# Kernel optimization log

Hardware: AMD Instinct MI355X
Metric: run time of the kernel (lower is better)

Reference implementation:

```python
import jax, jax.numpy as jnp
import numpy as np

N, IN_RAW, H, E, UNROLLS = 1024, 10, 96, 16384, 2

def _p(key, shape):
    return jax.random.normal(key, shape, dtype=jnp.float32) * 0.05

def setup_inputs() -> dict:
    key = jax.random.key(0)
    ks = jax.random.split(key, 24)
    x = jax.random.normal(ks[0], (N, IN_RAW), dtype=jnp.float32)
    edge_index = jax.random.randint(ks[1], (2, E), 0, N, dtype=jnp.int64)
    adj = jax.random.randint(ks[2], (N, N), 0, 2, dtype=jnp.int32)
    return {
        'x': x, 'edge_index': edge_index, 'adj': adj,
        # init_layer
        'W_init': _p(ks[3], (H, IN_RAW - 1)), 'b_init': _p(ks[4], (H,)),
        # GatedGraphConv (num_layers=1): weight [H,H], GRUCell params
        'W_ggc': _p(ks[5], (H, H)),
        'W_ih': _p(ks[6], (3 * H, H)), 'W_hh': _p(ks[7], (3 * H, H)),
        'b_ih': _p(ks[8], (3 * H,)), 'b_hh': _p(ks[9], (3 * H,)),
        # edge_attention: Linear(2H->H), Linear(H->1)
        'Wa1': _p(ks[10], (H, 2 * H)), 'ba1': _p(ks[11], (H,)),
        'Wa2': _p(ks[12], (1, H)), 'ba2': _p(ks[13], (1,)),
        # out MLP
        'Wo1': _p(ks[14], (H, H)), 'bo1': _p(ks[15], (H,)),
        'Wo2': _p(ks[16], (H, H)), 'bo2': _p(ks[17], (H,)),
        # heads
        'Wp1': _p(ks[18], (1, H)), 'bp1': _p(ks[19], (1,)),
        'Wp2': _p(ks[20], (1, H)), 'bp2': _p(ks[21], (1,)),
    }

def _leaky(v):
    return jnp.where(v >= 0, v, 0.01 * v)  # LeakyReLU default slope

def _ggnn_forward(x, edge_index, adj,
                  W_init, b_init, W_ggc, W_ih, W_hh, b_ih, b_hh,
                  Wa1, ba1, Wa2, ba2, Wo1, bo1, Wo2, bo2,
                  Wp1, bp1, Wp2, bp2):
    src, tgt = edge_index[0], edge_index[1]
    x = x[:, :-1]                                   # data.x[:, :-1]
    x = _leaky(x @ W_init.T + b_init)               # [N,H]
    adj_mask = (adj == 1)
    for _ in range(UNROLLS):
        # GatedGraphConv, 1 layer, aggr='mean'
        m = x @ W_ggc                               # [N,H]
        s = jax.ops.segment_sum(m[src], tgt, num_segments=N)
        cnt = jax.ops.segment_sum(jnp.ones((E,), x.dtype), tgt, num_segments=N)
        agg = s / jnp.maximum(cnt, 1.0)[:, None]    # mean, 0 for isolated nodes
        # GRUCell(agg, x)
        gi = agg @ W_ih.T + b_ih
        gh = x @ W_hh.T + b_hh
        ir, iz, inn = jnp.split(gi, 3, axis=1)
        hr, hz, hn = jnp.split(gh, 3, axis=1)
        r = jax.nn.sigmoid(ir + hr)
        z = jax.nn.sigmoid(iz + hz)
        n = jnp.tanh(inn + r * hn)
        x = (1.0 - z) * n + z * x
        # edge attention: concat(x_i, x_j) -> Linear(2H->H) decomposed into
        # two [H,H] halves so the NxNx2H concat tensor is never materialized.
        hi = x @ Wa1[:, :H].T                       # acts on t1 (row i)
        hj = x @ Wa1[:, H:].T                       # acts on t2 (row j)
        h = jax.nn.sigmoid(hi[:, None, :] + hj[None, :, :] + ba1)  # [N,N,H]
        coeffs = jax.nn.sigmoid(h @ Wa2[0] + ba2[0])               # [N,N]
        coeffs = jnp.where(adj_mask, coeffs, 0.0)
        x = coeffs @ x
    x = _leaky(x @ Wo1.T + bo1)
    x = _leaky(x @ Wo2.T + bo2)
    out1 = jax.nn.sigmoid(x @ Wp1.T + bp1)
    out2 = jax.nn.sigmoid(x @ Wp2.T + bp2)
    return out1, out2

def reference(x, edge_index, adj,
              W_init, b_init, W_ggc, W_ih, W_hh, b_ih, b_hh,
              Wa1, ba1, Wa2, ba2, Wo1, bo1, Wo2, bo2,
              Wp1, bp1, Wp2, bp2):
    return _ggnn_forward(x, edge_index, adj,
                         W_init, b_init, W_ggc, W_ih, W_hh, b_ih, b_hh,
                         Wa1, ba1, Wa2, ba2, Wo1, bo1, Wo2, bo2,
                         Wp1, bp1, Wp2, bp2)
```

## Files before the change

### kernel.cpp

```cpp
#include <hip/hip_runtime.h>

#define Nn 1024
#define Hh 96
#define Ee 16384
#define IN_K 9
#define IN_STRIDE 10
#define NH (Nn * Hh)
#define XS 128
#define SLOTS 64

__device__ __forceinline__ float sigf(float v) {
    return __builtin_amdgcn_rcpf(1.0f + __expf(-v));
}
__device__ __forceinline__ float tanhfast(float v) {
    float e = __expf(2.0f * v);
    return (e - 1.0f) * __builtin_amdgcn_rcpf(e + 1.0f);
}
__device__ __forceinline__ float leakyf(float v) {
    return v >= 0.0f ? v : 0.01f * v;
}

__global__ __launch_bounds__(256) void setup_kernel(
    const float* __restrict__ W_hh, const float* __restrict__ Wa1,
    const float* __restrict__ Wo1, const float* __restrict__ Wo2,
    const float* __restrict__ W_ggc, const float* __restrict__ W_ih,
    const float* __restrict__ x_in, const float* __restrict__ W_init,
    const float* __restrict__ b_init,
    float* __restrict__ Wt_hh, float* __restrict__ Wt_a1i,
    float* __restrict__ Wt_a1j, float* __restrict__ Wt_o1,
    float* __restrict__ Wt_o2, float* __restrict__ Wf,
    int* __restrict__ deg, float* __restrict__ xA)
{
    int gt = blockIdx.x * 256 + threadIdx.x;
    if (gt < Nn) deg[gt] = 0;
    if (gt < 64512) {
        int idx = gt;
        if (idx < 27648) {
            int k = idx / 288, c = idx % 288;
            Wt_hh[idx] = W_hh[c * 96 + k];
        } else if ((idx -= 27648) < 9216) {
            int k = idx / 96, h = idx % 96;
            Wt_a1i[idx] = Wa1[h * 192 + k];
        } else if ((idx -= 9216) < 9216) {
            int k = idx / 96, h = idx % 96;
            Wt_a1j[idx] = Wa1[h * 192 + 96 + k];
        } else if ((idx -= 9216) < 9216) {
            int k = idx / 96, j = idx % 96;
            Wt_o1[idx] = Wo1[j * 96 + k];
        } else {
            idx -= 9216;
            int k = idx / 96, j = idx % 96;
            Wt_o2[idx] = Wo2[j * 96 + k];
        }
    }
    if (gt < 27648) {
        int k = gt / 288, c = gt % 288;
        const float* g = W_ggc + k * 96;
        const float* w = W_ih + c * 96;
        float acc = 0.0f;
        for (int j = 0; j < 96; ++j) acc += g[j] * w[j];
        Wf[gt] = acc;
    }
    if (gt < NH) {
        int n = gt / Hh, j = gt - n * Hh;
        const float* xr = x_in + n * IN_STRIDE;
        const float* wr = W_init + j * IN_K;
        float acc = b_init[j];
#pragma unroll
        for (int k = 0; k < IN_K; ++k) acc += xr[k] * wr[k];
        xA[n * XS + j] = leakyf(acc);
    }
}

__global__ __launch_bounds__(256) void edges_kernel(
    const int* __restrict__ ei, int* __restrict__ deg, int* __restrict__ bucket)
{
    int e = blockIdx.x * 256 + threadIdx.x;
    if (e >= Ee) return;
    int src = ei[e];
    int tgt = ei[Ee + e];
    int slot = atomicAdd(&deg[tgt], 1);
    if (slot < SLOTS) bucket[tgt * SLOTS + slot] = src;
}

__global__ __launch_bounds__(384, 4) void gru_kernel(
    const float* __restrict__ xA, const int* __restrict__ deg,
    const int* __restrict__ bucket,
    const float* __restrict__ Wf, const float* __restrict__ Wt_hh,
    const float* __restrict__ b_ih, const float* __restrict__ b_hh,
    const float* __restrict__ Wt_a1i, const float* __restrict__ Wt_a1j,
    const float* __restrict__ ba1,
    float* __restrict__ xB, float* __restrict__ Ei, float* __restrict__ EjT)
{
    __shared__ float Pq[4][Hh];
    __shared__ float Pm[Hh];
    __shared__ float Xr[Hh];
    __shared__ float Xo[Hh];
    __shared__ float red6[4][Hh][6];
    __shared__ float redp[4][Hh][2];
    int tid = threadIdx.x;
    int q = tid / Hh;
    int h = tid - q * Hh;
    int n = blockIdx.x;
    {
        int d = deg[n];
        int dc = d < SLOTS ? d : SLOTS;
        const int* bk = bucket + n * SLOTS;
        float acc = 0.0f;
        for (int s = q; s < dc; s += 4)
            acc += xA[bk[s] * XS + h];
        Pq[q][h] = acc;
        if (q == 0) Xr[h] = xA[n * XS + h];
    }
    __syncthreads();
    if (q == 0) {
        float inv = __builtin_amdgcn_rcpf(fmaxf((float)deg[n], 1.0f));
        Pm[h] = (Pq[0][h] + Pq[1][h] + Pq[2][h] + Pq[3][h]) * inv;
    }
    __syncthreads();
    {
        const float* pf = Wf + h;
        const float* ph = Wt_hh + h;
        float gir = 0.f, giz = 0.f, gin = 0.f;
        float ghr = 0.f, ghz = 0.f, ghn = 0.f;
        int k0 = q * 24;
#pragma unroll 4
        for (int k = k0; k < k0 + 24; ++k) {
            float a = Pm[k];
            float xv = Xr[k];
            int o = k * 288;
            gir += a * pf[o];
            giz += a * pf[o + 96];
            gin += a * pf[o + 192];
            ghr += xv * ph[o];
            ghz += xv * ph[o + 96];
            ghn += xv * ph[o + 192];
        }
        red6[q][h][0] = gir;
        red6[q][h][1] = giz;
        red6[q][h][2] = gin;
        red6[q][h][3] = ghr;
        red6[q][h][4] = ghz;
        red6[q][h][5] = ghn;
    }
    __syncthreads();
    if (q == 0) {
        float gir = b_ih[h], giz = b_ih[Hh + h], gin = b_ih[2 * Hh + h];
        float ghr = b_hh[h], ghz = b_hh[Hh + h], ghn = b_hh[2 * Hh + h];
#pragma unroll
        for (int qq = 0; qq < 4; ++qq) {
            gir += red6[qq][h][0];
            giz += red6[qq][h][1];
            gin += red6[qq][h][2];
            ghr += red6[qq][h][3];
            ghz += red6[qq][h][4];
            ghn += red6[qq][h][5];
        }
        float rr = sigf(gir + ghr);
        float z = sigf(giz + ghz);
        float nn2 = tanhfast(gin + rr * ghn);
        float xo = (1.0f - z) * nn2 + z * Xr[h];
        xB[n * XS + h] = xo;
        Xo[h] = xo;
    }
    __syncthreads();
    {
        const float* wi = Wt_a1i + h;
        const float* wj = Wt_a1j + h;
        float a = 0.0f, bb = 0.0f;
        int k0 = q * 24;
#pragma unroll 4
        for (int k = k0; k < k0 + 24; ++k) {
            float xv = Xo[k];
            a += xv * wi[k * 96];
            bb += xv * wj[k * 96];
        }
        redp[q][h][0] = a;
        redp[q][h][1] = bb;
    }
    __syncthreads();
    if (q == 0) {
        float a = redp[0][h][0] + redp[1][h][0] + redp[2][h][0] + redp[3][h][0];
        float bb = redp[0][h][1] + redp[1][h][1] + redp[2][h][1] + redp[3][h][1];
        Ei[n * Hh + h] = __expf(-(a + ba1[h]));
        EjT[h * Nn + n] = __expf(-bb);
    }
}

__global__ __launch_bounds__(1024) void attn_kernel_u0(
    const float* __restrict__ Ei, const float* __restrict__ EjT,
    const float* __restrict__ Wa2, const float* __restrict__ ba2,
    const int* __restrict__ adj, const float* __restrict__ xB,
    float* __restrict__ xOut)
{
    __shared__ float sm[7168];
    int tid = threadIdx.x;
    int i0 = blockIdx.x * 4;
    {
        int j = tid;
        int m0 = adj[(i0 + 0) * Nn + j];
        int m1 = adj[(i0 + 1) * Nn + j];
        int m2 = adj[(i0 + 2) * Nn + j];
        int m3 = adj[(i0 + 3) * Nn + j];
        const float* e0 = Ei + i0 * Hh;
        float s0 = 0.f, s1 = 0.f, s2 = 0.f, s3 = 0.f;
#pragma unroll 8
        for (int k = 0; k < Hh; ++k) {
            float e = EjT[k * Nn + j];
            float wk = Wa2[k];
            s0 += __builtin_amdgcn_rcpf(fmaf(e0[k], e, 1.0f)) * wk;
            s1 += __builtin_amdgcn_rcpf(fmaf(e0[96 + k], e, 1.0f)) * wk;
            s2 += __builtin_amdgcn_rcpf(fmaf(e0[192 + k], e, 1.0f)) * wk;
            s3 += __builtin_amdgcn_rcpf(fmaf(e0[288 + k], e, 1.0f)) * wk;
        }
        float b2 = ba2[0];
        sm[0 * Nn + j] = (m0 == 1) ? sigf(s0 + b2) : 0.0f;
        sm[1 * Nn + j] = (m1 == 1) ? sigf(s1 + b2) : 0.0f;
        sm[2 * Nn + j] = (m2 == 1) ? sigf(s2 + b2) : 0.0f;
        sm[3 * Nn + j] = (m3 == 1) ? sigf(s3 + b2) : 0.0f;
    }
    __syncthreads();
    {
        int q = tid >> 7;
        int h = tid & 127;
        if (h < Hh) {
            int jb = q * 128;
            const float* xc = xB + jb * XS + h;
            const float* c0 = sm + 0 * Nn + jb;
            const float* c1 = sm + 1 * Nn + jb;
            const float* c2 = sm + 2 * Nn + jb;
            const float* c3 = sm + 3 * Nn + jb;
            float a0 = 0.f, a1 = 0.f, a2 = 0.f, a3 = 0.f;
#pragma unroll 4
            for (int j = 0; j < 128; ++j) {
                float xv = xc[j * XS];
                a0 += c0[j] * xv;
                a1 += c1[j] * xv;
                a2 += c2[j] * xv;
                a3 += c3[j] * xv;
            }
            sm[4096 + ((q * 4 + 0) * Hh) + h] = a0;
            sm[4096 + ((q * 4 + 1) * Hh) + h] = a1;
            sm[4096 + ((q * 4 + 2) * Hh) + h] = a2;
            sm[4096 + ((q * 4 + 3) * Hh) + h] = a3;
        }
    }
    __syncthreads();
    if (tid < 4 * Hh) {
        int r = tid / Hh, h = tid - r * Hh;
        float v = 0.f;
#pragma unroll
        for (int q = 0; q < 8; ++q)
            v += sm[4096 + ((q * 4 + r) * Hh) + h];
        xOut[(i0 + r) * XS + h] = v;
    }
}

__global__ __launch_bounds__(1024) void attn_kernel_u1(
    const float* __restrict__ Ei, const float* __restrict__ EjT,
    const float* __restrict__ Wa2, const float* __restrict__ ba2,
    const int* __restrict__ adj, const float* __restrict__ xB,
    const float* __restrict__ Wt_o1, const float* __restrict__ bo1,
    const float* __restrict__ Wt_o2, const float* __restrict__ bo2,
    const float* __restrict__ Wp1, const float* __restrict__ bp1,
    const float* __restrict__ Wp2, const float* __restrict__ bp2,
    float* __restrict__ out)
{
    __shared__ float sm[7168];
    __shared__ float hd[3][4][Hh];
    int tid = threadIdx.x;
    int i0 = blockIdx.x * 4;
    {
        int j = tid;
        int m0 = adj[(i0 + 0) * Nn + j];
        int m1 = adj[(i0 + 1) * Nn + j];
        int m2 = adj[(i0 + 2) * Nn + j];
        int m3 = adj[(i0 + 3) * Nn + j];
        const float* e0 = Ei + i0 * Hh;
        float s0 = 0.f, s1 = 0.f, s2 = 0.f, s3 = 0.f;
#pragma unroll 8
        for (int k = 0; k < Hh; ++k) {
            float e = EjT[k * Nn + j];
            float wk = Wa2[k];
            s0 += __builtin_amdgcn_rcpf(fmaf(e0[k], e, 1.0f)) * wk;
            s1 += __builtin_amdgcn_rcpf(fmaf(e0[96 + k], e, 1.0f)) * wk;
            s2 += __builtin_amdgcn_rcpf(fmaf(e0[192 + k], e, 1.0f)) * wk;
            s3 += __builtin_amdgcn_rcpf(fmaf(e0[288 + k], e, 1.0f)) * wk;
        }
        float b2 = ba2[0];
        sm[0 * Nn + j] = (m0 == 1) ? sigf(s0 + b2) : 0.0f;
        sm[1 * Nn + j] = (m1 == 1) ? sigf(s1 + b2) : 0.0f;
        sm[2 * Nn + j] = (m2 == 1) ? sigf(s2 + b2) : 0.0f;
        sm[3 * Nn + j] = (m3 == 1) ? sigf(s3 + b2) : 0.0f;
    }
    __syncthreads();
    {
        int q = tid >> 7;
        int h = tid & 127;
        if (h < Hh) {
            int jb = q * 128;
            const float* xc = xB + jb * XS + h;
            const float* c0 = sm + 0 * Nn + jb;
            const float* c1 = sm + 1 * Nn + jb;
            const float* c2 = sm + 2 * Nn + jb;
            const float* c3 = sm + 3 * Nn + jb;
            float a0 = 0.f, a1 = 0.f, a2 = 0.f, a3 = 0.f;
#pragma unroll 4
            for (int j = 0; j < 128; ++j) {
                float xv = xc[j * XS];
                a0 += c0[j] * xv;
                a1 += c1[j] * xv;
                a2 += c2[j] * xv;
                a3 += c3[j] * xv;
            }
            sm[4096 + ((q * 4 + 0) * Hh) + h] = a0;
            sm[4096 + ((q * 4 + 1) * Hh) + h] = a1;
            sm[4096 + ((q * 4 + 2) * Hh) + h] = a2;
            sm[4096 + ((q * 4 + 3) * Hh) + h] = a3;
        }
    }
    __syncthreads();
    if (tid < 4 * Hh) {
        int r = tid / Hh, h = tid - r * Hh;
        float v = 0.f;
#pragma unroll
        for (int q = 0; q < 8; ++q)
            v += sm[4096 + ((q * 4 + r) * Hh) + h];
        hd[0][r][h] = v;
    }
    __syncthreads();
    if (tid < 4 * Hh) {
        int r = tid / Hh, h = tid - r * Hh;
        const float* w = Wt_o1 + h;
        const float* xr = hd[0][r];
        float acc = bo1[h];
        for (int k = 0; k < Hh; ++k) acc += xr[k] * w[k * 96];
        hd[1][r][h] = leakyf(acc);
    }
    __syncthreads();
    if (tid < 4 * Hh) {
        int r = tid / Hh, h = tid - r * Hh;
        const float* w = Wt_o2 + h;
        const float* xr = hd[1][r];
        float acc = bo2[h];
        for (int k = 0; k < Hh; ++k) acc += xr[k] * w[k * 96];
        hd[2][r][h] = leakyf(acc);
    }
    __syncthreads();
    if (tid < 8) {
        int r = tid >> 1, which = tid & 1;
        const float* wp = which ? Wp2 : Wp1;
        const float* xr = hd[2][r];
        float acc = 0.f;
        for (int k = 0; k < Hh; ++k) acc += xr[k] * wp[k];
        float b = which ? bp2[0] : bp1[0];
        out[which * Nn + i0 + r] = sigf(acc + b);
    }
}

extern "C" void kernel_launch(void* const* d_in, const int* in_sizes, int n_in,
                              void* d_out, int out_size, void* d_ws, size_t ws_size,
                              hipStream_t stream)
{
    const float* x_in   = (const float*)d_in[0];
    const int*   ei     = (const int*)d_in[1];
    const int*   adj    = (const int*)d_in[2];
    const float* W_init = (const float*)d_in[3];
    const float* b_init = (const float*)d_in[4];
    const float* W_ggc  = (const float*)d_in[5];
    const float* W_ih   = (const float*)d_in[6];
    const float* W_hh   = (const float*)d_in[7];
    const float* b_ih   = (const float*)d_in[8];
    const float* b_hh   = (const float*)d_in[9];
    const float* Wa1    = (const float*)d_in[10];
    const float* ba1    = (const float*)d_in[11];
    const float* Wa2    = (const float*)d_in[12];
    const float* ba2    = (const float*)d_in[13];
    const float* Wo1    = (const float*)d_in[14];
    const float* bo1    = (const float*)d_in[15];
    const float* Wo2    = (const float*)d_in[16];
    const float* bo2    = (const float*)d_in[17];
    const float* Wp1    = (const float*)d_in[18];
    const float* bp1    = (const float*)d_in[19];
    const float* Wp2    = (const float*)d_in[20];
    const float* bp2    = (const float*)d_in[21];
    float* out = (float*)d_out;

    float* ws     = (float*)d_ws;
    float* xA     = ws;
    float* xB     = xA + Nn * XS;
    float* xC     = xB + Nn * XS;
    float* Ei     = xC + Nn * XS;
    float* EjT    = Ei + NH;
    float* Wt_hh  = EjT + NH;
    float* Wf     = Wt_hh + 27648;
    float* Wt_a1i = Wf + 27648;
    float* Wt_a1j = Wt_a1i + 9216;
    float* Wt_o1  = Wt_a1j + 9216;
    float* Wt_o2  = Wt_o1 + 9216;
    int*   deg    = (int*)(Wt_o2 + 9216);
    int*   bucket = deg + Nn;

    setup_kernel<<<(NH + 255) / 256, 256, 0, stream>>>(
        W_hh, Wa1, Wo1, Wo2, W_ggc, W_ih, x_in, W_init, b_init,
        Wt_hh, Wt_a1i, Wt_a1j, Wt_o1, Wt_o2, Wf, deg, xA);
    edges_kernel<<<(Ee + 255) / 256, 256, 0, stream>>>(ei, deg, bucket);

    gru_kernel<<<Nn, 384, 0, stream>>>(
        xA, deg, bucket, Wf, Wt_hh, b_ih, b_hh, Wt_a1i, Wt_a1j, ba1,
        xB, Ei, EjT);
    attn_kernel_u0<<<Nn / 4, 1024, 0, stream>>>(
        Ei, EjT, Wa2, ba2, adj, xB, xC);
    gru_kernel<<<Nn, 384, 0, stream>>>(
        xC, deg, bucket, Wf, Wt_hh, b_ih, b_hh, Wt_a1i, Wt_a1j, ba1,
        xB, Ei, EjT);
    attn_kernel_u1<<<Nn / 4, 1024, 0, stream>>>(
        Ei, EjT, Wa2, ba2, adj, xB,
        Wt_o1, bo1, Wt_o2, bo2, Wp1, bp1, Wp2, bp2, out);
}
```

Baseline: 192.7 us.

## Fuse all stages into one persistent kernel with global atomic barriers

Replaces the six separate launches (setup, edge bucketing, two GRU and two attention kernels) with a single 256-block persistent kernel that separates phases with atomic grid-wide barriers. The GRU phase now processes four nodes per block so each weight load is reused across four rows, and edge bucketing runs in one block using LDS atomics. This removes launch gaps and inter-kernel drain, at the cost of relying on all 256 blocks being co-resident, using only 384 of 1024 threads in the GRU phase, and adding a memset launch to reset the barrier counters.

```diff
diff --git a/kernel.cpp b/kernel.cpp
--- a/kernel.cpp
+++ b/kernel.cpp
@@ -8,6 +8,7 @@
 #define NH (Nn * Hh)
 #define XS 128
 #define SLOTS 64
+#define NBLK 256
 
 __device__ __forceinline__ float sigf(float v) {
     return __builtin_amdgcn_rcpf(1.0f + __expf(-v));
@@ -20,204 +21,189 @@
     return v >= 0.0f ? v : 0.01f * v;
 }
 
-__global__ __launch_bounds__(256) void setup_kernel(
-    const float* __restrict__ W_hh, const float* __restrict__ Wa1,
-    const float* __restrict__ Wo1, const float* __restrict__ Wo2,
-    const float* __restrict__ W_ggc, const float* __restrict__ W_ih,
-    const float* __restrict__ x_in, const float* __restrict__ W_init,
-    const float* __restrict__ b_init,
-    float* __restrict__ Wt_hh, float* __restrict__ Wt_a1i,
-    float* __restrict__ Wt_a1j, float* __restrict__ Wt_o1,
-    float* __restrict__ Wt_o2, float* __restrict__ Wf,
-    int* __restrict__ deg, float* __restrict__ xA)
-{
-    int gt = blockIdx.x * 256 + threadIdx.x;
-    if (gt < Nn) deg[gt] = 0;
-    if (gt < 64512) {
-        int idx = gt;
-        if (idx < 27648) {
-            int k = idx / 288, c = idx % 288;
-            Wt_hh[idx] = W_hh[c * 96 + k];
-        } else if ((idx -= 27648) < 9216) {
-            int k = idx / 96, h = idx % 96;
-            Wt_a1i[idx] = Wa1[h * 192 + k];
-        } else if ((idx -= 9216) < 9216) {
-            int k = idx / 96, h = idx % 96;
-            Wt_a1j[idx] = Wa1[h * 192 + 96 + k];
-        } else if ((idx -= 9216) < 9216) {
-            int k = idx / 96, j = idx % 96;
-            Wt_o1[idx] = Wo1[j * 96 + k];
-        } else {
-            idx -= 9216;
-            int k = idx / 96, j = idx % 96;
-            Wt_o2[idx] = Wo2[j * 96 + k];
-        }
-    }
-    if (gt < 27648) {
-        int k = gt / 288, c = gt % 288;
-        const float* g = W_ggc + k * 96;
-        const float* w = W_ih + c * 96;
+struct Params {
+    const float* x_in; const int* ei; const int* adj;
+    const float* W_init; const float* b_init;
+    const float* W_ggc; const float* W_ih; const float* W_hh;
+    const float* b_ih; const float* b_hh;
+    const float* Wa1; const float* ba1; const float* Wa2; const float* ba2;
+    const float* Wo1; const float* bo1; const float* Wo2; const float* bo2;
+    const float* Wp1; const float* bp1; const float* Wp2; const float* bp2;
+    float* out;
+    float* xA; float* xB; float* xC; float* Ei; float* EjT;
+    float* Wt_hh; float* Wf; float* Wt_a1i; float* Wt_a1j;
+    float* Wt_o1; float* Wt_o2;
+    int* deg; int* bucket; int* bar;
+};
+
+union Shm {
+    struct {
+        float Pm[4][Hh];
+        float Xr[4][Hh];
+        float Xo[4][Hh];
+        float red[4][4][6][Hh];
+        float redp[4][4][2][Hh];
+    } g;
+    struct {
+        float sm[7168];
+        float hd[3][4][Hh];
+    } a;
+    int ldeg[Nn];
+};
+
+__device__ __forceinline__ void gsync(int* bar, int idx) {
+    __syncthreads();
+    if (threadIdx.x == 0) {
+        __threadfence();
+        __hip_atomic_fetch_add(bar + idx, 1, __ATOMIC_ACQ_REL,
+                               __HIP_MEMORY_SCOPE_AGENT);
+        while (__hip_atomic_load(bar + idx, __ATOMIC_ACQUIRE,
+                                 __HIP_MEMORY_SCOPE_AGENT) < NBLK) {
+            __builtin_amdgcn_s_sleep(1);
+        }
+    }
+    __syncthreads();
+}
+
+__device__ __forceinline__ void gru_phase(const Params& p, Shm& sh,
+                                          const float* xin, float* xout)
+{
+    int tid = threadIdx.x;
+    int i0 = blockIdx.x * 4;
+    int h = tid % Hh;
+    int q = tid / Hh;
+    bool act = tid < 4 * Hh;
+
+    if (act) {
+        int n = i0 + q;
+        int d = p.deg[n];
+        int dc = d < SLOTS ? d : SLOTS;
+        const int* bk = p.bucket + n * SLOTS;
         float acc = 0.0f;
-        for (int j = 0; j < 96; ++j) acc += g[j] * w[j];
-        Wf[gt] = acc;
-    }
-    if (gt < NH) {
-        int n = gt / Hh, j = gt - n * Hh;
-        const float* xr = x_in + n * IN_STRIDE;
-        const float* wr = W_init + j * IN_K;
-        float acc = b_init[j];
-#pragma unroll
-        for (int k = 0; k < IN_K; ++k) acc += xr[k] * wr[k];
-        xA[n * XS + j] = leakyf(acc);
-    }
-}
-
-__global__ __launch_bounds__(256) void edges_kernel(
-    const int* __restrict__ ei, int* __restrict__ deg, int* __restrict__ bucket)
-{
-    int e = blockIdx.x * 256 + threadIdx.x;
-    if (e >= Ee) return;
-    int src = ei[e];
-    int tgt = ei[Ee + e];
-    int slot = atomicAdd(&deg[tgt], 1);
-    if (slot < SLOTS) bucket[tgt * SLOTS + slot] = src;
-}
-
-__global__ __launch_bounds__(384, 4) void gru_kernel(
-    const float* __restrict__ xA, const int* __restrict__ deg,
-    const int* __restrict__ bucket,
-    const float* __restrict__ Wf, const float* __restrict__ Wt_hh,
-    const float* __restrict__ b_ih, const float* __restrict__ b_hh,
-    const float* __restrict__ Wt_a1i, const float* __restrict__ Wt_a1j,
-    const float* __restrict__ ba1,
-    float* __restrict__ xB, float* __restrict__ Ei, float* __restrict__ EjT)
-{
-    __shared__ float Pq[4][Hh];
-    __shared__ float Pm[Hh];
-    __shared__ float Xr[Hh];
-    __shared__ float Xo[Hh];
-    __shared__ float red6[4][Hh][6];
-    __shared__ float redp[4][Hh][2];
-    int tid = threadIdx.x;
-    int q = tid / Hh;
-    int h = tid - q * Hh;
-    int n = blockIdx.x;
-    {
-        int d = deg[n];
-        int dc = d < SLOTS ? d : SLOTS;
-        const int* bk = bucket + n * SLOTS;
-        float acc = 0.0f;
-        for (int s = q; s < dc; s += 4)
-            acc += xA[bk[s] * XS + h];
-        Pq[q][h] = acc;
-        if (q == 0) Xr[h] = xA[n * XS + h];
-    }
-    __syncthreads();
-    if (q == 0) {
-        float inv = __builtin_amdgcn_rcpf(fmaxf((float)deg[n], 1.0f));
-        Pm[h] = (Pq[0][h] + Pq[1][h] + Pq[2][h] + Pq[3][h]) * inv;
-    }
-    __syncthreads();
-    {
-        const float* pf = Wf + h;
-        const float* ph = Wt_hh + h;
-        float gir = 0.f, giz = 0.f, gin = 0.f;
-        float ghr = 0.f, ghz = 0.f, ghn = 0.f;
+        for (int s = 0; s < dc; ++s)
+            acc += xin[bk[s] * XS + h];
+        float inv = __builtin_amdgcn_rcpf(fmaxf((float)d, 1.0f));
+        sh.g.Pm[q][h] = acc * inv;
+        sh.g.Xr[q][h] = xin[n * XS + h];
+    }
+    __syncthreads();
+
+    if (act) {
+        float g0[4], g1[4], g2[4], g3[4], g4[4], g5[4];
+#pragma unroll
+        for (int r = 0; r < 4; ++r) {
+            g0[r] = g1[r] = g2[r] = g3[r] = g4[r] = g5[r] = 0.0f;
+        }
+        const float* pf = p.Wf + h;
+        const float* ph = p.Wt_hh + h;
         int k0 = q * 24;
 #pragma unroll 4
         for (int k = k0; k < k0 + 24; ++k) {
-            float a = Pm[k];
-            float xv = Xr[k];
             int o = k * 288;
-            gir += a * pf[o];
-            giz += a * pf[o + 96];
-            gin += a * pf[o + 192];
-            ghr += xv * ph[o];
-            ghz += xv * ph[o + 96];
-            ghn += xv * ph[o + 192];
-        }
-        red6[q][h][0] = gir;
-        red6[q][h][1] = giz;
-        red6[q][h][2] = gin;
-        red6[q][h][3] = ghr;
-        red6[q][h][4] = ghz;
-        red6[q][h][5] = ghn;
-    }
-    __syncthreads();
-    if (q == 0) {
-        float gir = b_ih[h], giz = b_ih[Hh + h], gin = b_ih[2 * Hh + h];
-        float ghr = b_hh[h], ghz = b_hh[Hh + h], ghn = b_hh[2 * Hh + h];
+            float w0 = pf[o], w1 = pf[o + 96], w2 = pf[o + 192];
+            float u0 = ph[o], u1 = ph[o + 96], u2 = ph[o + 192];
+#pragma unroll
+            for (int r = 0; r < 4; ++r) {
+                float a  = sh.g.Pm[r][k];
+                float xv = sh.g.Xr[r][k];
+                g0[r] += a * w0;  g1[r] += a * w1;  g2[r] += a * w2;
+                g3[r] += xv * u0; g4[r] += xv * u1; g5[r] += xv * u2;
+            }
+        }
+#pragma unroll
+        for (int r = 0; r < 4; ++r) {
+            sh.g.red[q][r][0][h] = g0[r];
+            sh.g.red[q][r][1][h] = g1[r];
+            sh.g.red[q][r][2][h] = g2[r];
+            sh.g.red[q][r][3][h] = g3[r];
+            sh.g.red[q][r][4][h] = g4[r];
+            sh.g.red[q][r][5][h] = g5[r];
+        }
+    }
+    __syncthreads();
+
+    if (act) {
+        int n = i0 + q;
+        float gir = p.b_ih[h], giz = p.b_ih[Hh + h], gin = p.b_ih[2 * Hh + h];
+        float ghr = p.b_hh[h], ghz = p.b_hh[Hh + h], ghn = p.b_hh[2 * Hh + h];
 #pragma unroll
         for (int qq = 0; qq < 4; ++qq) {
-            gir += red6[qq][h][0];
-            giz += red6[qq][h][1];
-            gin += red6[qq][h][2];
-            ghr += red6[qq][h][3];
-            ghz += red6[qq][h][4];
-            ghn += red6[qq][h][5];
-        }
-        float rr = sigf(gir + ghr);
-        float z = sigf(giz + ghz);
+            gir += sh.g.red[qq][q][0][h];
+            giz += sh.g.red[qq][q][1][h];
+            gin += sh.g.red[qq][q][2][h];
+            ghr += sh.g.red[qq][q][3][h];
+            ghz += sh.g.red[qq][q][4][h];
+            ghn += sh.g.red[qq][q][5][h];
+        }
+        float rr  = sigf(gir + ghr);
+        float z   = sigf(giz + ghz);
         float nn2 = tanhfast(gin + rr * ghn);
-        float xo = (1.0f - z) * nn2 + z * Xr[h];
-        xB[n * XS + h] = xo;
-        Xo[h] = xo;
-    }
-    __syncthreads();
-    {
-        const float* wi = Wt_a1i + h;
-        const float* wj = Wt_a1j + h;
-        float a = 0.0f, bb = 0.0f;
+        float xo  = (1.0f - z) * nn2 + z * sh.g.Xr[q][h];
+        xout[n * XS + h] = xo;
+        sh.g.Xo[q][h] = xo;
+    }
+    __syncthreads();
+
+    if (act) {
+        const float* wi = p.Wt_a1i + h;
+        const float* wj = p.Wt_a1j + h;
+        float pa[4] = {0, 0, 0, 0}, pb[4] = {0, 0, 0, 0};
         int k0 = q * 24;
 #pragma unroll 4
         for (int k = k0; k < k0 + 24; ++k) {
-            float xv = Xo[k];
-            a += xv * wi[k * 96];
-            bb += xv * wj[k * 96];
-        }
-        redp[q][h][0] = a;
-        redp[q][h][1] = bb;
-    }
-    __syncthreads();
-    if (q == 0) {
-        float a = redp[0][h][0] + redp[1][h][0] + redp[2][h][0] + redp[3][h][0];
-        float bb = redp[0][h][1] + redp[1][h][1] + redp[2][h][1] + redp[3][h][1];
-        Ei[n * Hh + h] = __expf(-(a + ba1[h]));
-        EjT[h * Nn + n] = __expf(-bb);
-    }
-}
-
-__global__ __launch_bounds__(1024) void attn_kernel_u0(
-    const float* __restrict__ Ei, const float* __restrict__ EjT,
-    const float* __restrict__ Wa2, const float* __restrict__ ba2,
-    const int* __restrict__ adj, const float* __restrict__ xB,
-    float* __restrict__ xOut)
-{
-    __shared__ float sm[7168];
+            float wik = wi[k * 96], wjk = wj[k * 96];
+#pragma unroll
+            for (int r = 0; r < 4; ++r) {
+                float xv = sh.g.Xo[r][k];
+                pa[r] += xv * wik;
+                pb[r] += xv * wjk;
+            }
+        }
+#pragma unroll
+        for (int r = 0; r < 4; ++r) {
+            sh.g.redp[q][r][0][h] = pa[r];
+            sh.g.redp[q][r][1][h] = pb[r];
+        }
+    }
+    __syncthreads();
+    if (act) {
+        int n = i0 + q;
+        float a = sh.g.redp[0][q][0][h] + sh.g.redp[1][q][0][h]
+                + sh.g.redp[2][q][0][h] + sh.g.redp[3][q][0][h];
+        float b = sh.g.redp[0][q][1][h] + sh.g.redp[1][q][1][h]
+                + sh.g.redp[2][q][1][h] + sh.g.redp[3][q][1][h];
+        p.Ei[n * Hh + h]  = __expf(-(a + p.ba1[h]));
+        p.EjT[h * Nn + n] = __expf(-b);
+    }
+}
+
+__device__ __forceinline__ void attn_coeff(const Params& p, Shm& sh,
+                                           const float* xB)
+{
     int tid = threadIdx.x;
     int i0 = blockIdx.x * 4;
     {
         int j = tid;
-        int m0 = adj[(i0 + 0) * Nn + j];
-        int m1 = adj[(i0 + 1) * Nn + j];
-        int m2 = adj[(i0 + 2) * Nn + j];
-        int m3 = adj[(i0 + 3) * Nn + j];
-        const float* e0 = Ei + i0 * Hh;
+        int m0 = p.adj[(i0 + 0) * Nn + j];
+        int m1 = p.adj[(i0 + 1) * Nn + j];
+        int m2 = p.adj[(i0 + 2) * Nn + j];
+        int m3 = p.adj[(i0 + 3) * Nn + j];
+        const float* e0 = p.Ei + i0 * Hh;
         float s0 = 0.f, s1 = 0.f, s2 = 0.f, s3 = 0.f;
 #pragma unroll 8
         for (int k = 0; k < Hh; ++k) {
-            float e = EjT[k * Nn + j];
-            float wk = Wa2[k];
+            float e = p.EjT[k * Nn + j];
+            float wk = p.Wa2[k];
             s0 += __builtin_amdgcn_rcpf(fmaf(e0[k], e, 1.0f)) * wk;
             s1 += __builtin_amdgcn_rcpf(fmaf(e0[96 + k], e, 1.0f)) * wk;
             s2 += __builtin_amdgcn_rcpf(fmaf(e0[192 + k], e, 1.0f)) * wk;
             s3 += __builtin_amdgcn_rcpf(fmaf(e0[288 + k], e, 1.0f)) * wk;
         }
-        float b2 = ba2[0];
-        sm[0 * Nn + j] = (m0 == 1) ? sigf(s0 + b2) : 0.0f;
-        sm[1 * Nn + j] = (m1 == 1) ? sigf(s1 + b2) : 0.0f;
-        sm[2 * Nn + j] = (m2 == 1) ? sigf(s2 + b2) : 0.0f;
-        sm[3 * Nn + j] = (m3 == 1) ? sigf(s3 + b2) : 0.0f;
+        float b2 = p.ba2[0];
+        sh.a.sm[0 * Nn + j] = (m0 == 1) ? sigf(s0 + b2) : 0.0f;
+        sh.a.sm[1 * Nn + j] = (m1 == 1) ? sigf(s1 + b2) : 0.0f;
+        sh.a.sm[2 * Nn + j] = (m2 == 1) ? sigf(s2 + b2) : 0.0f;
+        sh.a.sm[3 * Nn + j] = (m3 == 1) ? sigf(s3 + b2) : 0.0f;
     }
     __syncthreads();
     {
@@ -226,10 +212,10 @@
         if (h < Hh) {
             int jb = q * 128;
             const float* xc = xB + jb * XS + h;
-            const float* c0 = sm + 0 * Nn + jb;
-            const float* c1 = sm + 1 * Nn + jb;
-            const float* c2 = sm + 2 * Nn + jb;
-            const float* c3 = sm + 3 * Nn + jb;
+            const float* c0 = sh.a.sm + 0 * Nn + jb;
+            const float* c1 = sh.a.sm + 1 * Nn + jb;
+            const float* c2 = sh.a.sm + 2 * Nn + jb;
+            const float* c3 = sh.a.sm + 3 * Nn + jb;
             float a0 = 0.f, a1 = 0.f, a2 = 0.f, a3 = 0.f;
 #pragma unroll 4
             for (int j = 0; j < 128; ++j) {
@@ -239,123 +225,141 @@
                 a2 += c2[j] * xv;
                 a3 += c3[j] * xv;
             }
-            sm[4096 + ((q * 4 + 0) * Hh) + h] = a0;
-            sm[4096 + ((q * 4 + 1) * Hh) + h] = a1;
-            sm[4096 + ((q * 4 + 2) * Hh) + h] = a2;
-            sm[4096 + ((q * 4 + 3) * Hh) + h] = a3;
-        }
-    }
-    __syncthreads();
+            sh.a.sm[4096 + ((q * 4 + 0) * Hh) + h] = a0;
+            sh.a.sm[4096 + ((q * 4 + 1) * Hh) + h] = a1;
+            sh.a.sm[4096 + ((q * 4 + 2) * Hh) + h] = a2;
+            sh.a.sm[4096 + ((q * 4 + 3) * Hh) + h] = a3;
+        }
+    }
+    __syncthreads();
+}
+
+__device__ __forceinline__ void attn_tail_u0(const Params& p, Shm& sh,
+                                             float* xOut)
+{
+    int tid = threadIdx.x;
+    int i0 = blockIdx.x * 4;
     if (tid < 4 * Hh) {
         int r = tid / Hh, h = tid - r * Hh;
         float v = 0.f;
 #pragma unroll
         for (int q = 0; q < 8; ++q)
-            v += sm[4096 + ((q * 4 + r) * Hh) + h];
+            v += sh.a.sm[4096 + ((q * 4 + r) * Hh) + h];
         xOut[(i0 + r) * XS + h] = v;
     }
 }
 
-__global__ __launch_bounds__(1024) void attn_kernel_u1(
-    const float* __restrict__ Ei, const float* __restrict__ EjT,
-    const float* __restrict__ Wa2, const float* __restrict__ ba2,
-    const int* __restrict__ adj, const float* __restrict__ xB,
-    const float* __restrict__ Wt_o1, const float* __restrict__ bo1,
-    const float* __restrict__ Wt_o2, const float* __restrict__ bo2,
-    const float* __restrict__ Wp1, const float* __restrict__ bp1,
-    const float* __restrict__ Wp2, const float* __restrict__ bp2,
-    float* __restrict__ out)
-{
-    __shared__ float sm[7168];
-    __shared__ float hd[3][4][Hh];
+__device__ __forceinline__ void attn_tail_u1(const Params& p, Shm& sh)
+{
     int tid = threadIdx.x;
     int i0 = blockIdx.x * 4;
-    {
-        int j = tid;
-        int m0 = adj[(i0 + 0) * Nn + j];
-        int m1 = adj[(i0 + 1) * Nn + j];
-        int m2 = adj[(i0 + 2) * Nn + j];
-        int m3 = adj[(i0 + 3) * Nn + j];
-        const float* e0 = Ei + i0 * Hh;
-        float s0 = 0.f, s1 = 0.f, s2 = 0.f, s3 = 0.f;
-#pragma unroll 8
-        for (int k = 0; k < Hh; ++k) {
-            float e = EjT[k * Nn + j];
-            float wk = Wa2[k];
-            s0 += __builtin_amdgcn_rcpf(fmaf(e0[k], e, 1.0f)) * wk;
-            s1 += __builtin_amdgcn_rcpf(fmaf(e0[96 + k], e, 1.0f)) * wk;
-            s2 += __builtin_amdgcn_rcpf(fmaf(e0[192 + k], e, 1.0f)) * wk;
-            s3 += __builtin_amdgcn_rcpf(fmaf(e0[288 + k], e, 1.0f)) * wk;
-        }
-        float b2 = ba2[0];
-        sm[0 * Nn + j] = (m0 == 1) ? sigf(s0 + b2) : 0.0f;
-        sm[1 * Nn + j] = (m1 == 1) ? sigf(s1 + b2) : 0.0f;
-        sm[2 * Nn + j] = (m2 == 1) ? sigf(s2 + b2) : 0.0f;
-        sm[3 * Nn + j] = (m3 == 1) ? sigf(s3 + b2) : 0.0f;
-    }
-    __syncthreads();
-    {
-        int q = tid >> 7;
-        int h = tid & 127;
-        if (h < Hh) {
-            int jb = q * 128;
-            const float* xc = xB + jb * XS + h;
-            const float* c0 = sm + 0 * Nn + jb;
-            const float* c1 = sm + 1 * Nn + jb;
-            const float* c2 = sm + 2 * Nn + jb;
-            const float* c3 = sm + 3 * Nn + jb;
-            float a0 = 0.f, a1 = 0.f, a2 = 0.f, a3 = 0.f;
-#pragma unroll 4
-            for (int j = 0; j < 128; ++j) {
-                float xv = xc[j * XS];
-                a0 += c0[j] * xv;
-                a1 += c1[j] * xv;
-                a2 += c2[j] * xv;
-                a3 += c3[j] * xv;
-            }
-            sm[4096 + ((q * 4 + 0) * Hh) + h] = a0;
-            sm[4096 + ((q * 4 + 1) * Hh) + h] = a1;
-            sm[4096 + ((q * 4 + 2) * Hh) + h] = a2;
-            sm[4096 + ((q * 4 + 3) * Hh) + h] = a3;
-        }
-    }
-    __syncthreads();
     if (tid < 4 * Hh) {
         int r = tid / Hh, h = tid - r * Hh;
         float v = 0.f;
 #pragma unroll
         for (int q = 0; q < 8; ++q)
-            v += sm[4096 + ((q * 4 + r) * Hh) + h];
-        hd[0][r][h] = v;
+            v += sh.a.sm[4096 + ((q * 4 + r) * Hh) + h];
+        sh.a.hd[0][r][h] = v;
     }
     __syncthreads();
     if (tid < 4 * Hh) {
         int r = tid / Hh, h = tid - r * Hh;
-        const float* w = Wt_o1 + h;
-        const float* xr = hd[0][r];
-        float acc = bo1[h];
+        const float* w = p.Wt_o1 + h;
+        const float* xr = sh.a.hd[0][r];
+        float acc = p.bo1[h];
         for (int k = 0; k < Hh; ++k) acc += xr[k] * w[k * 96];
-        hd[1][r][h] = leakyf(acc);
+        sh.a.hd[1][r][h] = leakyf(acc);
     }
     __syncthreads();
     if (tid < 4 * Hh) {
         int r = tid / Hh, h = tid - r * Hh;
-        const float* w = Wt_o2 + h;
-        const float* xr = hd[1][r];
-        float acc = bo2[h];
+        const float* w = p.Wt_o2 + h;
+        const float* xr = sh.a.hd[1][r];
+        float acc = p.bo2[h];
         for (int k = 0; k < Hh; ++k) acc += xr[k] * w[k * 96];
-        hd[2][r][h] = leakyf(acc);
+        sh.a.hd[2][r][h] = leakyf(acc);
     }
     __syncthreads();
     if (tid < 8) {
         int r = tid >> 1, which = tid & 1;
-        const float* wp = which ? Wp2 : Wp1;
-        const float* xr = hd[2][r];
+        const float* wp = which ? p.Wp2 : p.Wp1;
+        const float* xr = sh.a.hd[2][r];
         float acc = 0.f;
         for (int k = 0; k < Hh; ++k) acc += xr[k] * wp[k];
-        float b = which ? bp2[0] : bp1[0];
-        out[which * Nn + i0 + r] = sigf(acc + b);
-    }
+        float b = which ? p.bp2[0] : p.bp1[0];
+        p.out[which * Nn + i0 + r] = sigf(acc + b);
+    }
+}
+
+__global__ __launch_bounds__(1024) void fused_kernel(Params p)
+{
+    __shared__ Shm sh;
+    int tid = threadIdx.x;
+    int blk = blockIdx.x;
+
+    if (blk == 0) {
+        sh.ldeg[tid] = 0;
+        __syncthreads();
+        for (int e = tid; e < Ee; e += 1024) {
+            int src = p.ei[e];
+            int tgt = p.ei[Ee + e];
+            int slot = atomicAdd(&sh.ldeg[tgt], 1);
+            if (slot < SLOTS) p.bucket[tgt * SLOTS + slot] = src;
+        }
+        __syncthreads();
+        p.deg[tid] = sh.ldeg[tid];
+    } else {
+        int gt = (blk - 1) * 1024 + tid;
+        if (gt < 64512) {
+            int idx = gt;
+            if (idx < 27648) {
+                int k = idx / 288, c = idx % 288;
+                p.Wt_hh[idx] = p.W_hh[c * 96 + k];
+            } else if ((idx -= 27648) < 9216) {
+                int k = idx / 96, h2 = idx % 96;
+                p.Wt_a1i[idx] = p.Wa1[h2 * 192 + k];
+            } else if ((idx -= 9216) < 9216) {
+                int k = idx / 96, h2 = idx % 96;
+                p.Wt_a1j[idx] = p.Wa1[h2 * 192 + 96 + k];
+            } else if ((idx -= 9216) < 9216) {
+                int k = idx / 96, j = idx % 96;
+                p.Wt_o1[idx] = p.Wo1[j * 96 + k];
+            } else {
+                idx -= 9216;
+                int k = idx / 96, j = idx % 96;
+                p.Wt_o2[idx] = p.Wo2[j * 96 + k];
+            }
+        }
+        if (gt < 27648) {
+            int k = gt / 288, c = gt % 288;
+            const float* g = p.W_ggc + k * 96;
+            const float* w = p.W_ih + c * 96;
+            float acc = 0.0f;
+            for (int j = 0; j < 96; ++j) acc += g[j] * w[j];
+            p.Wf[gt] = acc;
+        }
+        if (gt < NH) {
+            int n = gt / Hh, j = gt - n * Hh;
+            const float* xr = p.x_in + n * IN_STRIDE;
+            const float* wr = p.W_init + j * IN_K;
+            float acc = p.b_init[j];
+#pragma unroll
+            for (int k = 0; k < IN_K; ++k) acc += xr[k] * wr[k];
+            p.xA[n * XS + j] = leakyf(acc);
+        }
+    }
+    gsync(p.bar, 0);
+
+    gru_phase(p, sh, p.xA, p.xB);
+    gsync(p.bar, 1);
+    attn_coeff(p, sh, p.xB);
+    attn_tail_u0(p, sh, p.xC);
+    gsync(p.bar, 2);
+
+    gru_phase(p, sh, p.xC, p.xB);
+    gsync(p.bar, 3);
+    attn_coeff(p, sh, p.xB);
+    attn_tail_u1(p, sh);
 }
 
 extern "C" void kernel_launch(void* const* d_in, const int* in_sizes, int n_in,
@@ -400,21 +404,23 @@
     float* Wt_o2  = Wt_o1 + 9216;
     int*   deg    = (int*)(Wt_o2 + 9216);
     int*   bucket = deg + Nn;
-
-    setup_kernel<<<(NH + 255) / 256, 256, 0, stream>>>(
-        W_hh, Wa1, Wo1, Wo2, W_ggc, W_ih, x_in, W_init, b_init,
-        Wt_hh, Wt_a1i, Wt_a1j, Wt_o1, Wt_o2, Wf, deg, xA);
-    edges_kernel<<<(Ee + 255) / 256, 256, 0, stream>>>(ei, deg, bucket);
-
-    gru_kernel<<<Nn, 384, 0, stream>>>(
-        xA, deg, bucket, Wf, Wt_hh, b_ih, b_hh, Wt_a1i, Wt_a1j, ba1,
-        xB, Ei, EjT);
-    attn_kernel_u0<<<Nn / 4, 1024, 0, stream>>>(
-        Ei, EjT, Wa2, ba2, adj, xB, xC);
-    gru_kernel<<<Nn, 384, 0, stream>>>(
-        xC, deg, bucket, Wf, Wt_hh, b_ih, b_hh, Wt_a1i, Wt_a1j, ba1,
-        xB, Ei, EjT);
-    attn_kernel_u1<<<Nn / 4, 1024, 0, stream>>>(
-        Ei, EjT, Wa2, ba2, adj, xB,
-        Wt_o1, bo1, Wt_o2, bo2, Wp1, bp1, Wp2, bp2, out);
-}
+    int*   bar    = bucket + Nn * SLOTS;
+
+    hipMemsetAsync(bar, 0, 4 * sizeof(int), stream);
+
+    Params p;
+    p.x_in = x_in; p.ei = ei; p.adj = adj;
+    p.W_init = W_init; p.b_init = b_init;
+    p.W_ggc = W_ggc; p.W_ih = W_ih; p.W_hh = W_hh;
+    p.b_ih = b_ih; p.b_hh = b_hh;
+    p.Wa1 = Wa1; p.ba1 = ba1; p.Wa2 = Wa2; p.ba2 = ba2;
+    p.Wo1 = Wo1; p.bo1 = bo1; p.Wo2 = Wo2; p.bo2 = bo2;
+    p.Wp1 = Wp1; p.bp1 = bp1; p.Wp2 = Wp2; p.bp2 = bp2;
+    p.out = out;
+    p.xA = xA; p.xB = xB; p.xC = xC; p.Ei = Ei; p.EjT = EjT;
+    p.Wt_hh = Wt_hh; p.Wf = Wf; p.Wt_a1i = Wt_a1i; p.Wt_a1j = Wt_a1j;
+    p.Wt_o1 = Wt_o1; p.Wt_o2 = Wt_o2;
+    p.deg = deg; p.bucket = bucket; p.bar = bar;
+
+    fused_kernel<<<NBLK, 1024, 0, stream>>>(p);
+}
```

Measured after the change: 449.1 us. 2.33x slower.

## Batch four nodes per GRU block, fuse edge bucketing into setup, stage attention operands

Applied to the files above, without the earlier changes.

The GRU kernel now handles four nodes per 768-thread block, so each weight load from Wf, Wt_hh and the attention projection matrices is reused across four rows instead of one. Edge bucketing moves into the setup kernel, using the spare threads of 1024-thread blocks, and a memset replaces the in-kernel zeroing of deg. That removes one launch but means setup must run after the memset. The attention kernels stage Ei rows and Wa2 in shared memory before the inner loop instead of re-reading them from global memory. The cost is fewer GRU blocks (256) with more threads and shared memory each, which lowers the number of blocks available to spread across the GPU.

```diff
diff --git a/kernel.cpp b/kernel.cpp
--- a/kernel.cpp
+++ b/kernel.cpp
@@ -20,30 +20,31 @@
     return v >= 0.0f ? v : 0.01f * v;
 }
 
-__global__ __launch_bounds__(256) void setup_kernel(
+__global__ __launch_bounds__(1024) void setup_kernel(
     const float* __restrict__ W_hh, const float* __restrict__ Wa1,
     const float* __restrict__ Wo1, const float* __restrict__ Wo2,
     const float* __restrict__ W_ggc, const float* __restrict__ W_ih,
     const float* __restrict__ x_in, const float* __restrict__ W_init,
-    const float* __restrict__ b_init,
+    const float* __restrict__ b_init, const int* __restrict__ ei,
     float* __restrict__ Wt_hh, float* __restrict__ Wt_a1i,
     float* __restrict__ Wt_a1j, float* __restrict__ Wt_o1,
     float* __restrict__ Wt_o2, float* __restrict__ Wf,
-    int* __restrict__ deg, float* __restrict__ xA)
+    float* __restrict__ xA, int* __restrict__ deg, int* __restrict__ bucket)
 {
-    int gt = blockIdx.x * 256 + threadIdx.x;
-    if (gt < Nn) deg[gt] = 0;
+    int tid = threadIdx.x;
+    int blk = blockIdx.x;
+    int gt = blk * 1024 + tid;
     if (gt < 64512) {
         int idx = gt;
         if (idx < 27648) {
             int k = idx / 288, c = idx % 288;
             Wt_hh[idx] = W_hh[c * 96 + k];
         } else if ((idx -= 27648) < 9216) {
-            int k = idx / 96, h = idx % 96;
-            Wt_a1i[idx] = Wa1[h * 192 + k];
+            int k = idx / 96, h2 = idx % 96;
+            Wt_a1i[idx] = Wa1[h2 * 192 + k];
         } else if ((idx -= 9216) < 9216) {
-            int k = idx / 96, h = idx % 96;
-            Wt_a1j[idx] = Wa1[h * 192 + 96 + k];
+            int k = idx / 96, h2 = idx % 96;
+            Wt_a1j[idx] = Wa1[h2 * 192 + 96 + k];
         } else if ((idx -= 9216) < 9216) {
             int k = idx / 96, j = idx % 96;
             Wt_o1[idx] = Wo1[j * 96 + k];
@@ -70,120 +71,130 @@
         for (int k = 0; k < IN_K; ++k) acc += xr[k] * wr[k];
         xA[n * XS + j] = leakyf(acc);
     }
-}
-
-__global__ __launch_bounds__(256) void edges_kernel(
-    const int* __restrict__ ei, int* __restrict__ deg, int* __restrict__ bucket)
-{
-    int e = blockIdx.x * 256 + threadIdx.x;
-    if (e >= Ee) return;
-    int src = ei[e];
-    int tgt = ei[Ee + e];
-    int slot = atomicAdd(&deg[tgt], 1);
-    if (slot < SLOTS) bucket[tgt * SLOTS + slot] = src;
-}
-
-__global__ __launch_bounds__(384, 4) void gru_kernel(
-    const float* __restrict__ xA, const int* __restrict__ deg,
+    if (tid >= 960) {
+        int e = blk * 64 + (tid - 960);
+        int src = ei[e];
+        int tgt = ei[Ee + e];
+        int slot = atomicAdd(&deg[tgt], 1);
+        if (slot < SLOTS) bucket[tgt * SLOTS + slot] = src;
+    }
+}
+
+struct GShm {
+    float Pg[2][4][Hh];
+    float Pm[4][Hh];
+    float Xr[4][Hh];
+    float Xo[4][Hh];
+    float gd[6][4][Hh];
+    float redp[2][4][4][Hh];
+};
+
+__global__ __launch_bounds__(768) void gru_kernel(
+    const float* __restrict__ xin, const int* __restrict__ deg,
     const int* __restrict__ bucket,
     const float* __restrict__ Wf, const float* __restrict__ Wt_hh,
     const float* __restrict__ b_ih, const float* __restrict__ b_hh,
     const float* __restrict__ Wt_a1i, const float* __restrict__ Wt_a1j,
     const float* __restrict__ ba1,
-    float* __restrict__ xB, float* __restrict__ Ei, float* __restrict__ EjT)
+    float* __restrict__ xout, float* __restrict__ Ei, float* __restrict__ EjT)
 {
-    __shared__ float Pq[4][Hh];
-    __shared__ float Pm[Hh];
-    __shared__ float Xr[Hh];
-    __shared__ float Xo[Hh];
-    __shared__ float red6[4][Hh][6];
-    __shared__ float redp[4][Hh][2];
+    __shared__ GShm sh;
     int tid = threadIdx.x;
-    int q = tid / Hh;
-    int h = tid - q * Hh;
-    int n = blockIdx.x;
-    {
+    int i0 = blockIdx.x * 4;
+
+    {
+        int h = tid % Hh;
+        int rr = (tid / Hh) & 3;
+        int s2 = tid / 384;
+        int n = i0 + rr;
         int d = deg[n];
         int dc = d < SLOTS ? d : SLOTS;
         const int* bk = bucket + n * SLOTS;
         float acc = 0.0f;
-        for (int s = q; s < dc; s += 4)
-            acc += xA[bk[s] * XS + h];
-        Pq[q][h] = acc;
-        if (q == 0) Xr[h] = xA[n * XS + h];
-    }
-    __syncthreads();
-    if (q == 0) {
-        float inv = __builtin_amdgcn_rcpf(fmaxf((float)deg[n], 1.0f));
-        Pm[h] = (Pq[0][h] + Pq[1][h] + Pq[2][h] + Pq[3][h]) * inv;
-    }
-    __syncthreads();
-    {
-        const float* pf = Wf + h;
-        const float* ph = Wt_hh + h;
-        float gir = 0.f, giz = 0.f, gin = 0.f;
-        float ghr = 0.f, ghz = 0.f, ghn = 0.f;
+        for (int s = s2; s < dc; s += 2)
+            acc += xin[bk[s] * XS + h];
+        sh.Pg[s2][rr][h] = acc;
+        if (s2 == 0) sh.Xr[rr][h] = xin[n * XS + h];
+    }
+    __syncthreads();
+    if (tid < 384) {
+        int h = tid % Hh, rr = tid / Hh;
+        float inv = __builtin_amdgcn_rcpf(fmaxf((float)deg[i0 + rr], 1.0f));
+        sh.Pm[rr][h] = (sh.Pg[0][rr][h] + sh.Pg[1][rr][h]) * inv;
+    }
+    __syncthreads();
+
+    if (tid < 576) {
+        int h = tid % Hh;
+        int g = tid / Hh;
+        bool ipath = g < 3;
+        int gc = ipath ? g : g - 3;
+        const float* W = (ipath ? Wf : Wt_hh) + gc * 96 + h;
+        const float (*src)[Hh] = ipath ? sh.Pm : sh.Xr;
+        float a0 = 0.f, a1 = 0.f, a2 = 0.f, a3 = 0.f;
+#pragma unroll 8
+        for (int k = 0; k < 96; ++k) {
+            float w = W[k * 288];
+            a0 += src[0][k] * w;
+            a1 += src[1][k] * w;
+            a2 += src[2][k] * w;
+            a3 += src[3][k] * w;
+        }
+        sh.gd[g][0][h] = a0;
+        sh.gd[g][1][h] = a1;
+        sh.gd[g][2][h] = a2;
+        sh.gd[g][3][h] = a3;
+    }
+    __syncthreads();
+
+    if (tid < 384) {
+        int h = tid % Hh, rr = tid / Hh;
+        float gir = b_ih[h]        + sh.gd[0][rr][h];
+        float giz = b_ih[96 + h]   + sh.gd[1][rr][h];
+        float gin = b_ih[192 + h]  + sh.gd[2][rr][h];
+        float ghr = b_hh[h]        + sh.gd[3][rr][h];
+        float ghz = b_hh[96 + h]   + sh.gd[4][rr][h];
+        float ghn = b_hh[192 + h]  + sh.gd[5][rr][h];
+        float r_  = sigf(gir + ghr);
+        float z   = sigf(giz + ghz);
+        float nn2 = tanhfast(gin + r_ * ghn);
+        float xo  = (1.0f - z) * nn2 + z * sh.Xr[rr][h];
+        xout[(i0 + rr) * XS + h] = xo;
+        sh.Xo[rr][h] = xo;
+    }
+    __syncthreads();
+
+    {
+        int h = tid % Hh;
+        int q = (tid / Hh) & 3;
+        int w = tid / 384;
+        const float* Wp = (w ? Wt_a1j : Wt_a1i) + h;
+        float a0 = 0.f, a1 = 0.f, a2 = 0.f, a3 = 0.f;
         int k0 = q * 24;
 #pragma unroll 4
         for (int k = k0; k < k0 + 24; ++k) {
-            float a = Pm[k];
-            float xv = Xr[k];
-            int o = k * 288;
-            gir += a * pf[o];
-            giz += a * pf[o + 96];
-            gin += a * pf[o + 192];
-            ghr += xv * ph[o];
-            ghz += xv * ph[o + 96];
-            ghn += xv * ph[o + 192];
-        }
-        red6[q][h][0] = gir;
-        red6[q][h][1] = giz;
-        red6[q][h][2] = gin;
-        red6[q][h][3] = ghr;
-        red6[q][h][4] = ghz;
-        red6[q][h][5] = ghn;
-    }
-    __syncthreads();
-    if (q == 0) {
-        float gir = b_ih[h], giz = b_ih[Hh + h], gin = b_ih[2 * Hh + h];
-        float ghr = b_hh[h], ghz = b_hh[Hh + h], ghn = b_hh[2 * Hh + h];
-#pragma unroll
-        for (int qq = 0; qq < 4; ++qq) {
-            gir += red6[qq][h][0];
-            giz += red6[qq][h][1];
-            gin += red6[qq][h][2];
-            ghr += red6[qq][h][3];
-            ghz += red6[qq][h][4];
-            ghn += red6[qq][h][5];
-        }
-        float rr = sigf(gir + ghr);
-        float z = sigf(giz + ghz);
-        float nn2 = tanhfast(gin + rr * ghn);
-        float xo = (1.0f - z) * nn2 + z * Xr[h];
-        xB[n * XS + h] = xo;
-        Xo[h] = xo;
-    }
-    __syncthreads();
-    {
-        const float* wi = Wt_a1i + h;
-        const float* wj = Wt_a1j + h;
-        float a = 0.0f, bb = 0.0f;
-        int k0 = q * 24;
-#pragma unroll 4
-        for (int k = k0; k < k0 + 24; ++k) {
-            float xv = Xo[k];
-            a += xv * wi[k * 96];
-            bb += xv * wj[k * 96];
-        }
-        redp[q][h][0] = a;
-        redp[q][h][1] = bb;
-    }
-    __syncthreads();
-    if (q == 0) {
-        float a = redp[0][h][0] + redp[1][h][0] + redp[2][h][0] + redp[3][h][0];
-        float bb = redp[0][h][1] + redp[1][h][1] + redp[2][h][1] + redp[3][h][1];
-        Ei[n * Hh + h] = __expf(-(a + ba1[h]));
-        EjT[h * Nn + n] = __expf(-bb);
+            float wv = Wp[k * 96];
+            a0 += sh.Xo[0][k] * wv;
+            a1 += sh.Xo[1][k] * wv;
+            a2 += sh.Xo[2][k] * wv;
+            a3 += sh.Xo[3][k] * wv;
+        }
+        sh.redp[w][q][0][h] = a0;
+        sh.redp[w][q][1][h] = a1;
+        sh.redp[w][q][2][h] = a2;
+        sh.redp[w][q][3][h] = a3;
+    }
+    __syncthreads();
+
+    {
+        int h = tid % Hh;
+        int rr = (tid / Hh) & 3;
+        int w = tid / 384;
+        int n = i0 + rr;
+        float s = sh.redp[w][0][rr][h] + sh.redp[w][1][rr][h]
+                + sh.redp[w][2][rr][h] + sh.redp[w][3][rr][h];
+        if (w == 0) Ei[n * Hh + h]  = __expf(-(s + ba1[h]));
+        else        EjT[h * Nn + n] = __expf(-s);
     }
 }
 
@@ -194,24 +205,28 @@
     float* __restrict__ xOut)
 {
     __shared__ float sm[7168];
+    __shared__ float eis[4 * Hh];
+    __shared__ float wa2s[Hh];
     int tid = threadIdx.x;
     int i0 = blockIdx.x * 4;
+    if (tid < 4 * Hh) eis[tid] = Ei[i0 * Hh + tid];
+    if (tid >= 512 && tid < 512 + Hh) wa2s[tid - 512] = Wa2[tid - 512];
     {
         int j = tid;
         int m0 = adj[(i0 + 0) * Nn + j];
         int m1 = adj[(i0 + 1) * Nn + j];
         int m2 = adj[(i0 + 2) * Nn + j];
         int m3 = adj[(i0 + 3) * Nn + j];
-        const float* e0 = Ei + i0 * Hh;
+        __syncthreads();
         float s0 = 0.f, s1 = 0.f, s2 = 0.f, s3 = 0.f;
 #pragma unroll 8
         for (int k = 0; k < Hh; ++k) {
             float e = EjT[k * Nn + j];
-            float wk = Wa2[k];
-            s0 += __builtin_amdgcn_rcpf(fmaf(e0[k], e, 1.0f)) * wk;
-            s1 += __builtin_amdgcn_rcpf(fmaf(e0[96 + k], e, 1.0f)) * wk;
-            s2 += __builtin_amdgcn_rcpf(fmaf(e0[192 + k], e, 1.0f)) * wk;
-            s3 += __builtin_amdgcn_rcpf(fmaf(e0[288 + k], e, 1.0f)) * wk;
+            float wk = wa2s[k];
+            s0 += __builtin_amdgcn_rcpf(fmaf(eis[k], e, 1.0f)) * wk;
+            s1 += __builtin_amdgcn_rcpf(fmaf(eis[96 + k], e, 1.0f)) * wk;
+            s2 += __builtin_amdgcn_rcpf(fmaf(eis[192 + k], e, 1.0f)) * wk;
+            s3 += __builtin_amdgcn_rcpf(fmaf(eis[288 + k], e, 1.0f)) * wk;
         }
         float b2 = ba2[0];
         sm[0 * Nn + j] = (m0 == 1) ? sigf(s0 + b2) : 0.0f;
@@ -267,25 +282,29 @@
     float* __restrict__ out)
 {
     __shared__ float sm[7168];
+    __shared__ float eis[4 * Hh];
+    __shared__ float wa2s[Hh];
     __shared__ float hd[3][4][Hh];
     int tid = threadIdx.x;
     int i0 = blockIdx.x * 4;
+    if (tid < 4 * Hh) eis[tid] = Ei[i0 * Hh + tid];
+    if (tid >= 512 && tid < 512 + Hh) wa2s[tid - 512] = Wa2[tid - 512];
     {
         int j = tid;
         int m0 = adj[(i0 + 0) * Nn + j];
         int m1 = adj[(i0 + 1) * Nn + j];
         int m2 = adj[(i0 + 2) * Nn + j];
         int m3 = adj[(i0 + 3) * Nn + j];
-        const float* e0 = Ei + i0 * Hh;
+        __syncthreads();
         float s0 = 0.f, s1 = 0.f, s2 = 0.f, s3 = 0.f;
 #pragma unroll 8
         for (int k = 0; k < Hh; ++k) {
             float e = EjT[k * Nn + j];
-            float wk = Wa2[k];
-            s0 += __builtin_amdgcn_rcpf(fmaf(e0[k], e, 1.0f)) * wk;
-            s1 += __builtin_amdgcn_rcpf(fmaf(e0[96 + k], e, 1.0f)) * wk;
-            s2 += __builtin_amdgcn_rcpf(fmaf(e0[192 + k], e, 1.0f)) * wk;
-            s3 += __builtin_amdgcn_rcpf(fmaf(e0[288 + k], e, 1.0f)) * wk;
+            float wk = wa2s[k];
+            s0 += __builtin_amdgcn_rcpf(fmaf(eis[k], e, 1.0f)) * wk;
+            s1 += __builtin_amdgcn_rcpf(fmaf(eis[96 + k], e, 1.0f)) * wk;
+            s2 += __builtin_amdgcn_rcpf(fmaf(eis[192 + k], e, 1.0f)) * wk;
+            s3 += __builtin_amdgcn_rcpf(fmaf(eis[288 + k], e, 1.0f)) * wk;
         }
         float b2 = ba2[0];
         sm[0 * Nn + j] = (m0 == 1) ? sigf(s0 + b2) : 0.0f;
@@ -401,20 +420,22 @@
     int*   deg    = (int*)(Wt_o2 + 9216);
     int*   bucket = deg + Nn;
 
-    setup_kernel<<<(NH + 255) / 256, 256, 0, stream>>>(
-        W_hh, Wa1, Wo1, Wo2, W_ggc, W_ih, x_in, W_init, b_init,
-        Wt_hh, Wt_a1i, Wt_a1j, Wt_o1, Wt_o2, Wf, deg, xA);
-    edges_kernel<<<(Ee + 255) / 256, 256, 0, stream>>>(ei, deg, bucket);
-
-    gru_kernel<<<Nn, 384, 0, stream>>>(
+    hipMemsetAsync(deg, 0, Nn * sizeof(int), stream);
+
+    setup_kernel<<<256, 1024, 0, stream>>>(
+        W_hh, Wa1, Wo1, Wo2, W_ggc, W_ih, x_in, W_init, b_init, ei,
+        Wt_hh, Wt_a1i, Wt_a1j, Wt_o1, Wt_o2, Wf, xA, deg, bucket);
+
+    gru_kernel<<<256, 768, 0, stream>>>(
         xA, deg, bucket, Wf, Wt_hh, b_ih, b_hh, Wt_a1i, Wt_a1j, ba1,
         xB, Ei, EjT);
-    attn_kernel_u0<<<Nn / 4, 1024, 0, stream>>>(
+    attn_kernel_u0<<<256, 1024, 0, stream>>>(
         Ei, EjT, Wa2, ba2, adj, xB, xC);
-    gru_kernel<<<Nn, 384, 0, stream>>>(
+
+    gru_kernel<<<256, 768, 0, stream>>>(
         xC, deg, bucket, Wf, Wt_hh, b_ih, b_hh, Wt_a1i, Wt_a1j, ba1,
         xB, Ei, EjT);
-    attn_kernel_u1<<<Nn / 4, 1024, 0, stream>>>(
+    attn_kernel_u1<<<256, 1024, 0, stream>>>(
         Ei, EjT, Wa2, ba2, adj, xB,
         Wt_o1, bo1, Wt_o2, bo2, Wp1, bp1, Wp2, bp2, out);
 }
```

New measurement: 196.1 us. No clear change (+1.8%).
